# Optimization experiments

Hardware: AMD Instinct MI355X
Metric: run time of the kernel (lower is better)

Reference implementation:

```python
import jax, jax.numpy as jnp
import numpy as np

N_NODES = 50000
HEADS = 16
HEAD_DIM = 8  # hidden_dim 128 / 16 heads
IN_DIM = 128
HID = HEADS * HEAD_DIM
NEG_SLOPE = 0.2


def setup_inputs() -> dict:
    key = jax.random.key(0)
    ks = jax.random.split(key, 12)
    s = 1.0 / np.sqrt(IN_DIM)
    s2 = 1.0 / np.sqrt(HID)
    return {
        "x": jax.random.normal(ks[0], (N_NODES, IN_DIM), jnp.float32),
        "edge_index": jax.random.randint(ks[1], (2, 800000), 0, N_NODES, jnp.int64),
        "W1": jax.random.normal(ks[2], (IN_DIM, HID), jnp.float32) * s,
        "a_src1": jax.random.normal(ks[3], (HEADS, HEAD_DIM), jnp.float32) * s,
        "a_dst1": jax.random.normal(ks[4], (HEADS, HEAD_DIM), jnp.float32) * s,
        "b1": jnp.zeros((HID,), jnp.float32),
        "W2": jax.random.normal(ks[5], (HID, HID), jnp.float32) * s2,
        "a_src2": jax.random.normal(ks[6], (HEADS, HEAD_DIM), jnp.float32) * s2,
        "a_dst2": jax.random.normal(ks[7], (HEADS, HEAD_DIM), jnp.float32) * s2,
        "b2": jnp.zeros((HID,), jnp.float32),
    }


def _gat_conv(x, src, dst, W, a_src, a_dst, bias):
    N = x.shape[0]
    xh = (x @ W).reshape(N, HEADS, HEAD_DIM)            # [N,H,C]
    al_s = jnp.einsum('nhc,hc->nh', xh, a_src)           # [N,H]
    al_d = jnp.einsum('nhc,hc->nh', xh, a_dst)           # [N,H]
    e = jax.nn.leaky_relu(al_s[src] + al_d[dst], NEG_SLOPE)  # [E,H]
    m = jax.ops.segment_max(e, dst, num_segments=N)      # per-dst max, [N,H]
    m = jnp.where(jnp.isfinite(m), m, 0.0)
    ex = jnp.exp(e - m[dst])
    denom = jax.ops.segment_sum(ex, dst, num_segments=N)
    alpha = ex / (denom[dst] + 1e-16)                    # [E,H]
    msg = xh[src] * alpha[:, :, None]                    # [E,H,C]
    out = jax.ops.segment_sum(msg, dst, num_segments=N)  # [N,H,C]
    return out.reshape(N, HID) + bias


def reference(x, edge_index, W1, a_src1, a_dst1, b1, W2, a_src2, a_dst2, b2):
    N = x.shape[0]
    # PyG GATConv default: add self-loops
    loops = jnp.arange(N, dtype=edge_index.dtype)
    src = jnp.concatenate([edge_index[0], loops])
    dst = jnp.concatenate([edge_index[1], loops])
    h = jax.nn.elu(_gat_conv(x, src, dst, W1, a_src1, a_dst1, b1))
    h = _gat_conv(h, src, dst, W2, a_src2, a_dst2, b2)
    return h
```

## Files before the change

kernel.cpp:

```cpp
#include <hip/hip_runtime.h>
#include <hip/hip_fp16.h>
#include <math.h>

#define DIM   128
#define HEADS 16
#define NEG   0.2f
#define GROWS 32

__global__ void k_detect(const void* __restrict__ ei, int* __restrict__ flag) {
    __shared__ int red[256];
    const int t = threadIdx.x;
    const int* p = (const int*)ei;
    int m = 0;
    for (int i = t; i < 4096; i += 256) m |= p[2 * i + 1];
    red[t] = m;
    __syncthreads();
    for (int off = 128; off > 0; off >>= 1) {
        if (t < off) red[t] |= red[t + off];
        __syncthreads();
    }
    if (t == 0) flag[0] = (red[0] == 0) ? 1 : 0;
}

__device__ __forceinline__ int edge_at(const void* ei, int is64, long long idx) {
    return is64 ? (int)((const long long*)ei)[idx] : ((const int*)ei)[idx];
}

__global__ __launch_bounds__(256) void k_gemm(const float* __restrict__ X,
                                              const float* __restrict__ W,
                                              const float* __restrict__ a_src,
                                              const float* __restrict__ a_dst,
                                              __half* __restrict__ XH16,
                                              __half* __restrict__ als16,
                                              float* __restrict__ ald,
                                              int N) {
    __shared__ float sW[DIM * DIM];
    __shared__ float sx[GROWS * DIM];
    const int t = threadIdx.x;
    const int row0 = blockIdx.x * GROWS;

    for (int i = t * 4; i < DIM * DIM; i += 256 * 4)
        *(float4*)&sW[i] = *(const float4*)&W[i];
    for (int i = t * 4; i < GROWS * DIM; i += 256 * 4) {
        const int r = row0 + (i >> 7);
        if (r < N) *(float4*)&sx[i] = *(const float4*)&X[(size_t)r * DIM + (i & 127)];
        else       *(float4*)&sx[i] = float4{0.f, 0.f, 0.f, 0.f};
    }
    __syncthreads();

    const int j0 = (t & 31) * 4;
    const int rr = (t >> 5) * 4;
    float4 a0 = {0,0,0,0}, a1 = {0,0,0,0}, a2 = {0,0,0,0}, a3 = {0,0,0,0};

    const float* sx0 = &sx[(rr + 0) * DIM];
    const float* sx1 = &sx[(rr + 1) * DIM];
    const float* sx2 = &sx[(rr + 2) * DIM];
    const float* sx3 = &sx[(rr + 3) * DIM];

#define MAC4(A, xv)                                                          \
    A.x += xv.x * w0.x + xv.y * w1.x + xv.z * w2.x + xv.w * w3.x;            \
    A.y += xv.x * w0.y + xv.y * w1.y + xv.z * w2.y + xv.w * w3.y;            \
    A.z += xv.x * w0.z + xv.y * w1.z + xv.z * w2.z + xv.w * w3.z;            \
    A.w += xv.x * w0.w + xv.y * w1.w + xv.z * w2.w + xv.w * w3.w;

#pragma unroll 4
    for (int k = 0; k < DIM; k += 4) {
        float4 x0 = *(const float4*)&sx0[k];
        float4 x1 = *(const float4*)&sx1[k];
        float4 x2 = *(const float4*)&sx2[k];
        float4 x3 = *(const float4*)&sx3[k];
        float4 w0 = *(const float4*)&sW[(k + 0) * DIM + j0];
        float4 w1 = *(const float4*)&sW[(k + 1) * DIM + j0];
        float4 w2 = *(const float4*)&sW[(k + 2) * DIM + j0];
        float4 w3 = *(const float4*)&sW[(k + 3) * DIM + j0];
        MAC4(a0, x0) MAC4(a1, x1) MAC4(a2, x2) MAC4(a3, x3)
    }
#undef MAC4

#pragma unroll
    for (int r = 0; r < 4; ++r) {
        const float4 ac = (r == 0) ? a0 : (r == 1) ? a1 : (r == 2) ? a2 : a3;
        const int row = row0 + rr + r;
        if (row < N) {
            __half2 p0 = __floats2half2_rn(ac.x, ac.y);
            __half2 p1 = __floats2half2_rn(ac.z, ac.w);
            uint2 pk;
            pk.x = *(unsigned*)&p0;
            pk.y = *(unsigned*)&p1;
            *(uint2*)&XH16[(size_t)row * DIM + j0] = pk;
        }
    }

    const int h = j0 >> 3;
    const float4 as4 = *(const float4*)&a_src[j0];
    const float4 ad4 = *(const float4*)&a_dst[j0];
#pragma unroll
    for (int r = 0; r < 4; ++r) {
        const float4 ac = (r == 0) ? a0 : (r == 1) ? a1 : (r == 2) ? a2 : a3;
        float s = ac.x * as4.x + ac.y * as4.y + ac.z * as4.z + ac.w * as4.w;
        float d = ac.x * ad4.x + ac.y * ad4.y + ac.z * ad4.z + ac.w * ad4.w;
        s += __shfl_xor(s, 1);
        d += __shfl_xor(d, 1);
        const int row = row0 + rr + r;
        if (((t & 1) == 0) && (row < N)) {
            als16[(size_t)row * HEADS + h] = __float2half_rn(s);
            ald[(size_t)row * HEADS + h]  = d;
        }
    }
}

__global__ void k_deg(const void* __restrict__ ei, const int* __restrict__ flag,
                      int* __restrict__ deg, int E0, int ET) {
    int e = blockIdx.x * 256 + threadIdx.x;
    if (e >= ET) return;
    int d = (e < E0) ? edge_at(ei, flag[0], (long long)E0 + e) : (e - E0);
    atomicAdd(&deg[d], 1);
}

__global__ void k_chunksum(const int* __restrict__ deg, int* __restrict__ csum, int N) {
    __shared__ int s[256];
    int t = threadIdx.x, i = blockIdx.x * 256 + t;
    s[t] = (i < N) ? deg[i] : 0;
    __syncthreads();
    for (int off = 128; off > 0; off >>= 1) { if (t < off) s[t] += s[t + off]; __syncthreads(); }
    if (t == 0) csum[blockIdx.x] = s[0];
}

__global__ void k_scantop(int* __restrict__ csum, int nch) {
    __shared__ int s[256];
    int t = threadIdx.x;
    int v = (t < nch) ? csum[t] : 0;
    s[t] = v;
    __syncthreads();
    for (int off = 1; off < 256; off <<= 1) {
        int x = (t >= off) ? s[t - off] : 0;
        __syncthreads();
        s[t] += x;
        __syncthreads();
    }
    if (t < nch) csum[t] = s[t] - v;
}

__global__ void k_scanadd(const int* __restrict__ deg, const int* __restrict__ csum,
                          int* __restrict__ rowptr, int* __restrict__ cur, int N) {
    __shared__ int s[256];
    int t = threadIdx.x, i = blockIdx.x * 256 + t;
    int v = (i < N) ? deg[i] : 0;
    s[t] = v;
    __syncthreads();
    for (int off = 1; off < 256; off <<= 1) {
        int x = (t >= off) ? s[t - off] : 0;
        __syncthreads();
        s[t] += x;
        __syncthreads();
    }
    if (i < N) { int ex = s[t] - v + csum[blockIdx.x]; rowptr[i] = ex; cur[i] = ex; }
}

__global__ void k_fill(const void* __restrict__ ei, const int* __restrict__ flag,
                       int* __restrict__ cur, int* __restrict__ ssrc, int E0, int ET) {
    int e = blockIdx.x * 256 + threadIdx.x;
    if (e >= ET) return;
    int is64 = flag[0];
    int s, d;
    if (e < E0) { s = edge_at(ei, is64, e); d = edge_at(ei, is64, (long long)E0 + e); }
    else        { s = d = e - E0; }
    int p = atomicAdd(&cur[d], 1);
    ssrc[p] = s;
}

__global__ __launch_bounds__(256) void k_edge(
    const int* __restrict__ rowptr, const int* __restrict__ deg,
    const int* __restrict__ ssrc,
    const __half* __restrict__ als16, const float* __restrict__ ald,
    const __half* __restrict__ XH16, const float* __restrict__ bias,
    float* __restrict__ out, int N, int DO_ELU)
{
    const int wv = threadIdx.x >> 6;
    const int lane = threadIdx.x & 63;
    const int node = blockIdx.x * 4 + wv;
    if (node >= N) return;

    const int start = rowptr[node];
    const int dg = deg[node];
    const int h = lane >> 2;
    const float aldh = ald[(size_t)node * HEADS + h];
    int myS = (lane < dg) ? ssrc[start + lane] : 0;

    float acc0 = 0.f, acc1 = 0.f, sum = 0.f;
#pragma unroll 8
    for (int k = 0; k < dg; ++k) {
        int s = (k < 64) ? __builtin_amdgcn_readlane(myS, k)
                         : ssrc[start + k];
        float e = __half2float(als16[(size_t)s * HEADS + h]) + aldh;
        e = (e > 0.f) ? e : NEG * e;
        float w = __expf(e);
        sum += w;
        float2 f = __half22float2(*(const __half2*)&XH16[(size_t)s * DIM + 2 * lane]);
        acc0 += w * f.x;
        acc1 += w * f.y;
    }
    const float inv = 1.f / (sum + 1e-16f);
    const float2 bias2 = *(const float2*)&bias[lane * 2];
    float v0 = acc0 * inv + bias2.x;
    float v1 = acc1 * inv + bias2.y;
    if (DO_ELU) {
        v0 = (v0 > 0.f) ? v0 : expm1f(v0);
        v1 = (v1 > 0.f) ? v1 : expm1f(v1);
    }
    *(float2*)&out[(size_t)node * DIM + lane * 2] = float2{v0, v1};
}

extern "C" void kernel_launch(void* const* d_in, const int* in_sizes, int n_in,
                              void* d_out, int out_size, void* d_ws, size_t ws_size,
                              hipStream_t stream) {
    const float* x      = (const float*)d_in[0];
    const void*  ei     = d_in[1];
    const float* W1     = (const float*)d_in[2];
    const float* a_src1 = (const float*)d_in[3];
    const float* a_dst1 = (const float*)d_in[4];
    const float* b1     = (const float*)d_in[5];
    const float* W2     = (const float*)d_in[6];
    const float* a_src2 = (const float*)d_in[7];
    const float* a_dst2 = (const float*)d_in[8];
    const float* b2     = (const float*)d_in[9];
    float* out = (float*)d_out;

    const int N  = in_sizes[0] / DIM;
    const int E0 = in_sizes[1] / 2;
    const int ET = E0 + N;

    float*  h1     = (float*)d_ws;
    float*  ald    = h1 + (size_t)N * DIM;
    __half* xh16   = (__half*)(ald + (size_t)N * HEADS);
    __half* als16  = xh16 + (size_t)N * DIM;
    int*    deg    = (int*)(als16 + (size_t)N * HEADS);
    int*    rowptr = deg + N;
    int*    cur    = rowptr + N;
    int*    csum   = cur + N;
    int*    flag   = csum + 256;
    int*    ssrc   = flag + 1;

    const int nch        = (N + 255) / 256;
    const int edgeBlocks = (ET + 255) / 256;
    const int gemmBlocks = (N + GROWS - 1) / GROWS;
    const int nodeBlocks = (N + 3) / 4;

    k_detect<<<1, 256, 0, stream>>>(ei, flag);
    hipMemsetAsync(deg, 0, (size_t)N * 4, stream);
    k_deg<<<edgeBlocks, 256, 0, stream>>>(ei, flag, deg, E0, ET);
    k_chunksum<<<nch, 256, 0, stream>>>(deg, csum, N);
    k_scantop<<<1, 256, 0, stream>>>(csum, nch);
    k_scanadd<<<nch, 256, 0, stream>>>(deg, csum, rowptr, cur, N);
    k_fill<<<edgeBlocks, 256, 0, stream>>>(ei, flag, cur, ssrc, E0, ET);

    k_gemm<<<gemmBlocks, 256, 0, stream>>>(x, W1, a_src1, a_dst1, xh16, als16, ald, N);
    k_edge<<<nodeBlocks, 256, 0, stream>>>(rowptr, deg, ssrc, als16, ald, xh16, b1, h1, N, 1);

    k_gemm<<<gemmBlocks, 256, 0, stream>>>(h1, W2, a_src2, a_dst2, xh16, als16, ald, N);
    k_edge<<<nodeBlocks, 256, 0, stream>>>(rowptr, deg, ssrc, als16, ald, xh16, b2, out, N, 0);
}
```

Baseline: 406.6 us.

## Replace CSR build with fixed-slot adjacency plus overflow list, batch attention weights

```diff
diff --git a/kernel.cpp b/kernel.cpp
--- a/kernel.cpp
+++ b/kernel.cpp
@@ -2,29 +2,12 @@
 #include <hip/hip_fp16.h>
 #include <math.h>
 
-#define DIM   128
-#define HEADS 16
-#define NEG   0.2f
-#define GROWS 32
-
-__global__ void k_detect(const void* __restrict__ ei, int* __restrict__ flag) {
-    __shared__ int red[256];
-    const int t = threadIdx.x;
-    const int* p = (const int*)ei;
-    int m = 0;
-    for (int i = t; i < 4096; i += 256) m |= p[2 * i + 1];
-    red[t] = m;
-    __syncthreads();
-    for (int off = 128; off > 0; off >>= 1) {
-        if (t < off) red[t] |= red[t + off];
-        __syncthreads();
-    }
-    if (t == 0) flag[0] = (red[0] == 0) ? 1 : 0;
-}
-
-__device__ __forceinline__ int edge_at(const void* ei, int is64, long long idx) {
-    return is64 ? (int)((const long long*)ei)[idx] : ((const int*)ei)[idx];
-}
+#define DIM     128
+#define HEADS   16
+#define NEG     0.2f
+#define GROWS   32
+#define SLOTS   56
+#define OVF_CAP 131072
 
 __global__ __launch_bounds__(256) void k_gemm(const float* __restrict__ X,
                                               const float* __restrict__ W,
@@ -33,11 +16,16 @@
                                               __half* __restrict__ XH16,
                                               __half* __restrict__ als16,
                                               float* __restrict__ ald,
-                                              int N) {
+                                              int N,
+                                              int* __restrict__ zero_buf,
+                                              int zero_n) {
     __shared__ float sW[DIM * DIM];
     __shared__ float sx[GROWS * DIM];
     const int t = threadIdx.x;
     const int row0 = blockIdx.x * GROWS;
+
+    const int gid = blockIdx.x * 256 + t;
+    if (zero_buf && gid < zero_n) zero_buf[gid] = 0;
 
     for (int i = t * 4; i < DIM * DIM; i += 256 * 4)
         *(float4*)&sW[i] = *(const float4*)&W[i];
@@ -109,101 +97,108 @@
     }
 }
 
-__global__ void k_deg(const void* __restrict__ ei, const int* __restrict__ flag,
-                      int* __restrict__ deg, int E0, int ET) {
-    int e = blockIdx.x * 256 + threadIdx.x;
+__global__ __launch_bounds__(256) void k_fill(const void* __restrict__ ei,
+                                              int* __restrict__ cnt,
+                                              int* __restrict__ ovf_cnt,
+                                              int* __restrict__ ssrc,
+                                              int* __restrict__ ovf,
+                                              int E0, int ET) {
+    __shared__ int sdet;
+    const int* p = (const int*)ei;
+    if (threadIdx.x < 64) {
+        int v = p[2 * threadIdx.x + 1];
+        unsigned long long b = __ballot(v != 0);
+        if (threadIdx.x == 0) sdet = (b == 0ULL) ? 1 : 0;
+    }
+    __syncthreads();
+    const int is64 = sdet;
+
+    const int e = blockIdx.x * 256 + threadIdx.x;
     if (e >= ET) return;
-    int d = (e < E0) ? edge_at(ei, flag[0], (long long)E0 + e) : (e - E0);
-    atomicAdd(&deg[d], 1);
-}
-
-__global__ void k_chunksum(const int* __restrict__ deg, int* __restrict__ csum, int N) {
-    __shared__ int s[256];
-    int t = threadIdx.x, i = blockIdx.x * 256 + t;
-    s[t] = (i < N) ? deg[i] : 0;
-    __syncthreads();
-    for (int off = 128; off > 0; off >>= 1) { if (t < off) s[t] += s[t + off]; __syncthreads(); }
-    if (t == 0) csum[blockIdx.x] = s[0];
-}
-
-__global__ void k_scantop(int* __restrict__ csum, int nch) {
-    __shared__ int s[256];
-    int t = threadIdx.x;
-    int v = (t < nch) ? csum[t] : 0;
-    s[t] = v;
-    __syncthreads();
-    for (int off = 1; off < 256; off <<= 1) {
-        int x = (t >= off) ? s[t - off] : 0;
-        __syncthreads();
-        s[t] += x;
-        __syncthreads();
-    }
-    if (t < nch) csum[t] = s[t] - v;
-}
-
-__global__ void k_scanadd(const int* __restrict__ deg, const int* __restrict__ csum,
-                          int* __restrict__ rowptr, int* __restrict__ cur, int N) {
-    __shared__ int s[256];
-    int t = threadIdx.x, i = blockIdx.x * 256 + t;
-    int v = (i < N) ? deg[i] : 0;
-    s[t] = v;
-    __syncthreads();
-    for (int off = 1; off < 256; off <<= 1) {
-        int x = (t >= off) ? s[t - off] : 0;
-        __syncthreads();
-        s[t] += x;
-        __syncthreads();
-    }
-    if (i < N) { int ex = s[t] - v + csum[blockIdx.x]; rowptr[i] = ex; cur[i] = ex; }
-}
-
-__global__ void k_fill(const void* __restrict__ ei, const int* __restrict__ flag,
-                       int* __restrict__ cur, int* __restrict__ ssrc, int E0, int ET) {
-    int e = blockIdx.x * 256 + threadIdx.x;
-    if (e >= ET) return;
-    int is64 = flag[0];
     int s, d;
-    if (e < E0) { s = edge_at(ei, is64, e); d = edge_at(ei, is64, (long long)E0 + e); }
-    else        { s = d = e - E0; }
-    int p = atomicAdd(&cur[d], 1);
-    ssrc[p] = s;
+    if (e < E0) {
+        if (is64) {
+            s = (int)((const long long*)ei)[e];
+            d = (int)((const long long*)ei)[(size_t)E0 + e];
+        } else {
+            s = ((const int*)ei)[e];
+            d = ((const int*)ei)[(size_t)E0 + e];
+        }
+    } else {
+        s = d = e - E0;
+    }
+    int pz = atomicAdd(&cnt[d], 1);
+    if (pz < SLOTS) {
+        ssrc[(size_t)d * SLOTS + pz] = s;
+    } else {
+        int o = atomicAdd(ovf_cnt, 1);
+        if (o < OVF_CAP) { ovf[2 * o] = s; ovf[2 * o + 1] = d; }
+    }
 }
 
 __global__ __launch_bounds__(256) void k_edge(
-    const int* __restrict__ rowptr, const int* __restrict__ deg,
-    const int* __restrict__ ssrc,
+    const int* __restrict__ cnt, const int* __restrict__ ssrc,
+    const int* __restrict__ ovf, const int* __restrict__ ovf_cnt,
     const __half* __restrict__ als16, const float* __restrict__ ald,
     const __half* __restrict__ XH16, const float* __restrict__ bias,
     float* __restrict__ out, int N, int DO_ELU)
 {
-    const int wv = threadIdx.x >> 6;
     const int lane = threadIdx.x & 63;
-    const int node = blockIdx.x * 4 + wv;
+    const int node = blockIdx.x * 4 + (threadIdx.x >> 6);
     if (node >= N) return;
 
-    const int start = rowptr[node];
-    const int dg = deg[node];
     const int h = lane >> 2;
+    const int q = lane & 3;
     const float aldh = ald[(size_t)node * HEADS + h];
-    int myS = (lane < dg) ? ssrc[start + lane] : 0;
-
-    float acc0 = 0.f, acc1 = 0.f, sum = 0.f;
-#pragma unroll 8
-    for (int k = 0; k < dg; ++k) {
-        int s = (k < 64) ? __builtin_amdgcn_readlane(myS, k)
-                         : ssrc[start + k];
-        float e = __half2float(als16[(size_t)s * HEADS + h]) + aldh;
-        e = (e > 0.f) ? e : NEG * e;
-        float w = __expf(e);
-        sum += w;
-        float2 f = __half22float2(*(const __half2*)&XH16[(size_t)s * DIM + 2 * lane]);
-        acc0 += w * f.x;
-        acc1 += w * f.y;
-    }
-    const float inv = 1.f / (sum + 1e-16f);
-    const float2 bias2 = *(const float2*)&bias[lane * 2];
-    float v0 = acc0 * inv + bias2.x;
-    float v1 = acc1 * inv + bias2.y;
+    const int dg  = cnt[node];
+    const int dgS = dg < SLOTS ? dg : SLOTS;
+    int myS = (lane < dgS) ? ssrc[(size_t)node * SLOTS + lane] : 0;
+    const int qb = (lane & ~3) << 2;
+
+    float acc0 = 0.f, acc1 = 0.f, sumW = 0.f;
+    const int ngrp = (dgS + 3) >> 2;
+    for (int g = 0; g < ngrp; ++g) {
+        const int kq = 4 * g + q;
+        int sL = __builtin_amdgcn_ds_bpermute(kq << 2, myS);
+        float a = __half2float(als16[(size_t)sL * HEADS + h]) + aldh;
+        a = (a > 0.f) ? a : NEG * a;
+        float w = (kq < dgS) ? __expf(a) : 0.f;
+        sumW += w;
+        const int wb = __float_as_int(w);
+#pragma unroll
+        for (int j = 0; j < 4; ++j) {
+            const int k = 4 * g + j;
+            if (k >= dgS) break;
+            float wj = __int_as_float(__builtin_amdgcn_ds_bpermute(qb + (j << 2), wb));
+            int sj = __builtin_amdgcn_readlane(myS, k);
+            float2 f = __half22float2(*(const __half2*)&XH16[(size_t)sj * DIM + 2 * lane]);
+            acc0 += wj * f.x;
+            acc1 += wj * f.y;
+        }
+    }
+    sumW += __shfl_xor(sumW, 1);
+    sumW += __shfl_xor(sumW, 2);
+
+    if (dg > SLOTS) {
+        int no = *ovf_cnt; if (no > OVF_CAP) no = OVF_CAP;
+        for (int i = 0; i < no; ++i) {
+            if (ovf[2 * i + 1] == node) {
+                int os = ovf[2 * i];
+                float a = __half2float(als16[(size_t)os * HEADS + h]) + aldh;
+                a = (a > 0.f) ? a : NEG * a;
+                float w = __expf(a);
+                sumW += w;
+                float2 f = __half22float2(*(const __half2*)&XH16[(size_t)os * DIM + 2 * lane]);
+                acc0 += w * f.x;
+                acc1 += w * f.y;
+            }
+        }
+    }
+
+    const float inv = 1.f / (sumW + 1e-16f);
+    const float2 b2 = *(const float2*)&bias[lane * 2];
+    float v0 = acc0 * inv + b2.x;
+    float v1 = acc1 * inv + b2.y;
     if (DO_ELU) {
         v0 = (v0 > 0.f) ? v0 : expm1f(v0);
         v1 = (v1 > 0.f) ? v1 : expm1f(v1);
@@ -230,33 +225,22 @@
     const int E0 = in_sizes[1] / 2;
     const int ET = E0 + N;
 
-    float*  h1     = (float*)d_ws;
-    float*  ald    = h1 + (size_t)N * DIM;
-    __half* xh16   = (__half*)(ald + (size_t)N * HEADS);
-    __half* als16  = xh16 + (size_t)N * DIM;
-    int*    deg    = (int*)(als16 + (size_t)N * HEADS);
-    int*    rowptr = deg + N;
-    int*    cur    = rowptr + N;
-    int*    csum   = cur + N;
-    int*    flag   = csum + 256;
-    int*    ssrc   = flag + 1;
-
-    const int nch        = (N + 255) / 256;
+    float*  h1      = (float*)d_ws;
+    float*  ald     = h1 + (size_t)N * DIM;
+    __half* xh16    = (__half*)(ald + (size_t)N * HEADS);
+    __half* als16   = xh16 + (size_t)N * DIM;
+    int*    cnt     = (int*)(als16 + (size_t)N * HEADS);
+    int*    ovf_cnt = cnt + N;
+    int*    ssrc    = ovf_cnt + 1;
+    int*    ovf     = ssrc + (size_t)N * SLOTS;
+
+    const int gemmBlocks = (N + GROWS - 1) / GROWS;
     const int edgeBlocks = (ET + 255) / 256;
-    const int gemmBlocks = (N + GROWS - 1) / GROWS;
     const int nodeBlocks = (N + 3) / 4;
 
-    k_detect<<<1, 256, 0, stream>>>(ei, flag);
-    hipMemsetAsync(deg, 0, (size_t)N * 4, stream);
-    k_deg<<<edgeBlocks, 256, 0, stream>>>(ei, flag, deg, E0, ET);
-    k_chunksum<<<nch, 256, 0, stream>>>(deg, csum, N);
-    k_scantop<<<1, 256, 0, stream>>>(csum, nch);
-    k_scanadd<<<nch, 256, 0, stream>>>(deg, csum, rowptr, cur, N);
-    k_fill<<<edgeBlocks, 256, 0, stream>>>(ei, flag, cur, ssrc, E0, ET);
-
-    k_gemm<<<gemmBlocks, 256, 0, stream>>>(x, W1, a_src1, a_dst1, xh16, als16, ald, N);
-    k_edge<<<nodeBlocks, 256, 0, stream>>>(rowptr, deg, ssrc, als16, ald, xh16, b1, h1, N, 1);
-
-    k_gemm<<<gemmBlocks, 256, 0, stream>>>(h1, W2, a_src2, a_dst2, xh16, als16, ald, N);
-    k_edge<<<nodeBlocks, 256, 0, stream>>>(rowptr, deg, ssrc, als16, ald, xh16, b2, out, N, 0);
-}
+    k_gemm<<<gemmBlocks, 256, 0, stream>>>(x, W1, a_src1, a_dst1, xh16, als16, ald, N, cnt, N + 1);
+    k_fill<<<edgeBlocks, 256, 0, stream>>>(ei, cnt, ovf_cnt, ssrc, ovf, E0, ET);
+    k_edge<<<nodeBlocks, 256, 0, stream>>>(cnt, ssrc, ovf, ovf_cnt, als16, ald, xh16, b1, h1, N, 1);
+    k_gemm<<<gemmBlocks, 256, 0, stream>>>(h1, W2, a_src2, a_dst2, xh16, als16, ald, N, nullptr, 0);
+    k_edge<<<nodeBlocks, 256, 0, stream>>>(cnt, ssrc, ovf, ovf_cnt, als16, ald, xh16, b2, out, N, 0);
+}
```

New measurement: 373.0 us. -8.3%, faster.
